# Kernel tuning notes

Hardware: AMD Instinct MI355X
Metric: run time of the kernel (lower is better)

The kernel has to match this reference:

```python
import jax, jax.numpy as jnp
import numpy as np

EPS = 1e-5

def _layernorm(x, w, b):
    mu = jnp.mean(x, axis=-1, keepdims=True)
    var = jnp.mean(jnp.square(x - mu), axis=-1, keepdims=True)
    return (x - mu) * jax.lax.rsqrt(var + EPS) * w + b

def setup_inputs() -> dict:
    key = jax.random.key(0)
    ks = jax.random.split(key, 8)
    B, N, C, D = 32, 1024, 4096, 64
    x = jax.random.normal(ks[0], (B, N, C), dtype=jnp.float32)
    gumbel = jax.random.gumbel(ks[1], (B, N, 2), dtype=jnp.float32)
    ln_w = jnp.ones((C,), jnp.float32)
    ln_b = jnp.zeros((C,), jnp.float32)
    w1 = jax.random.normal(ks[2], (C, D), dtype=jnp.float32) * 0.02
    b1 = jnp.zeros((D,), jnp.float32)
    w2 = jax.random.normal(ks[3], (D, 2), dtype=jnp.float32) * 0.02
    b2 = jnp.zeros((2,), jnp.float32)
    return {"x": x, "gumbel": gumbel, "ln_w": ln_w, "ln_b": ln_b,
            "w1": w1, "b1": b1, "w2": w2, "b2": b2}

def reference(x, gumbel, ln_w, ln_b, w1, b1, w2, b2):
    B, N, C = x.shape
    xn = _layernorm(x, ln_w, ln_b)
    local_x = xn[:, :, : C // 2]                      # [B, N, C/2]
    # policy is all-ones -> weighted mean over tokens
    global_x = jnp.mean(xn[:, :, C // 2:], axis=1, keepdims=True)  # [B, 1, C/2]
    feat = jnp.concatenate(
        [local_x, jnp.broadcast_to(global_x, local_x.shape)], axis=-1)  # [B, N, C]
    h = jax.nn.gelu(feat @ w1 + b1, approximate=False)  # [B, N, 64]
    logits = h @ w2 + b2                                # [B, N, 2]
    pred_score = jax.nn.log_softmax(logits, axis=-1)
    # gumbel-softmax (tau=1, hard=True) with straight-through estimator
    y_soft = jax.nn.softmax(pred_score + gumbel, axis=-1)
    hard = jax.nn.one_hot(jnp.argmax(y_soft, axis=-1), 2, dtype=y_soft.dtype)
    y = hard - jax.lax.stop_gradient(y_soft) + y_soft
    keep = y[:, :, 0]                                   # [B, N]
    # dense equivalent of masked_select/split: zero out dropped tokens
    return x * keep[:, :, None]
```

## Files before the change

kernel.cpp:

```cpp
#include <hip/hip_runtime.h>
#include <math.h>

#define B_   32
#define N_   1024
#define C_   4096
#define HC_  2048
#define D_   64
#define NT_  32768
#define BKC_ 64
#define NCH_ (HC_ / BKC_)
#define AST_ 68

__device__ __forceinline__ float4 ld4(const float* p) {
    return *reinterpret_cast<const float4*>(p);
}

__global__ __launch_bounds__(256) void mk1(
        const float* __restrict__ x, const float* __restrict__ lnw,
        const float* __restrict__ lnb, const float* __restrict__ w1,
        float* __restrict__ Pp, float* __restrict__ muv,
        float* __restrict__ rsv, float* __restrict__ part) {
    __shared__ float smem[8448];
    __shared__ float sLow[64], qLow[64];
    float* As = smem;
    float* Bsm = smem + 4352;

    const int t = threadIdx.x;
    const int tid = blockIdx.x;
    const int T0 = tid * 64;
    const int row = t >> 2;
    const int fq = t & 3;
    const int lane = t & 63, w = t >> 6;
    const int rt = lane >> 3, dt = lane & 7;

    float acc[64];
#pragma unroll
    for (int i = 0; i < 64; ++i) acc[i] = 0.f;
    float sR = 0.f, qR = 0.f;

    float4 xv[4];
    float4 wv[4];
    float lw[4];
    {
        const float* rp = x + (size_t)(T0 + row) * C_ + fq * 16;
#pragma unroll
        for (int i = 0; i < 4; ++i) xv[i] = ld4(rp + i * 4);
        const float4* s4 = reinterpret_cast<const float4*>(w1);
#pragma unroll
        for (int i = 0; i < 4; ++i) {
            wv[i] = s4[i * 256 + t];
            lw[i] = lnw[(i * 256 + t) >> 4];
        }
    }

#pragma unroll 1
    for (int c = 0; c < NCH_; ++c) {
#pragma unroll
        for (int i = 0; i < 4; ++i) {
            const float4 v = xv[i];
            const int kl = fq * 16 + i * 4;
            As[(kl + 0) * AST_ + row] = v.x;
            As[(kl + 1) * AST_ + row] = v.y;
            As[(kl + 2) * AST_ + row] = v.z;
            As[(kl + 3) * AST_ + row] = v.w;
            sR += (v.x + v.y) + (v.z + v.w);
            qR = fmaf(v.x, v.x, fmaf(v.y, v.y,
                 fmaf(v.z, v.z, fmaf(v.w, v.w, qR))));
        }
        {
            float4* b4 = reinterpret_cast<float4*>(Bsm);
#pragma unroll
            for (int i = 0; i < 4; ++i) {
                float4 v = wv[i];
                v.x *= lw[i]; v.y *= lw[i]; v.z *= lw[i]; v.w *= lw[i];
                b4[i * 256 + t] = v;
            }
        }
        __syncthreads();
        if (c + 1 < NCH_) {
            const int k1 = (c + 1) * BKC_;
            const float* rp = x + (size_t)(T0 + row) * C_ + k1 + fq * 16;
#pragma unroll
            for (int i = 0; i < 4; ++i) xv[i] = ld4(rp + i * 4);
            const float4* s4 = reinterpret_cast<const float4*>(
                w1 + (size_t)k1 * D_);
#pragma unroll
            for (int i = 0; i < 4; ++i) {
                wv[i] = s4[i * 256 + t];
                lw[i] = lnw[k1 + ((i * 256 + t) >> 4)];
            }
        }
#pragma unroll 8
        for (int kk = 0; kk < 16; ++kk) {
            const int k = w * 16 + kk;
            const float4 a0 = *reinterpret_cast<const float4*>(
                As + k * AST_ + rt * 8);
            const float4 a1 = *reinterpret_cast<const float4*>(
                As + k * AST_ + rt * 8 + 4);
            const float4 b0 = *reinterpret_cast<const float4*>(
                Bsm + k * 64 + dt * 8);
            const float4 b1 = *reinterpret_cast<const float4*>(
                Bsm + k * 64 + dt * 8 + 4);
            const float av[8] = {a0.x, a0.y, a0.z, a0.w,
                                 a1.x, a1.y, a1.z, a1.w};
            const float bv[8] = {b0.x, b0.y, b0.z, b0.w,
                                 b1.x, b1.y, b1.z, b1.w};
#pragma unroll
            for (int ri = 0; ri < 8; ++ri)
#pragma unroll
                for (int cj = 0; cj < 8; ++cj)
                    acc[ri * 8 + cj] =
                        fmaf(av[ri], bv[cj], acc[ri * 8 + cj]);
        }
        __syncthreads();
    }
    sR += __shfl_xor(sR, 1); qR += __shfl_xor(qR, 1);
    sR += __shfl_xor(sR, 2); qR += __shfl_xor(qR, 2);
    if (fq == 0) { sLow[row] = sR; qLow[row] = qR; }

#pragma unroll
    for (int h = 0; h < 2; ++h) {
#pragma unroll
        for (int i = 0; i < 32; ++i) smem[i * 256 + t] = acc[h * 32 + i];
        __syncthreads();
        if ((w >> 1) == h) {
#pragma unroll
            for (int r2 = 0; r2 < 2; ++r2) {
                const int rowO = rt * 8 + w * 2 + r2;
                float v[8];
#pragma unroll
                for (int cj = 0; cj < 8; ++cj) {
                    const int i = (w - 2 * h) * 16 + r2 * 8 + cj;
                    v[cj] = (smem[i * 256 + lane]
                             + smem[i * 256 + 64 + lane])
                          + (smem[i * 256 + 128 + lane]
                             + smem[i * 256 + 192 + lane]);
                }
                float* dst = Pp + (size_t)(T0 + rowO) * D_ + dt * 8;
                *reinterpret_cast<float4*>(dst) =
                    make_float4(v[0], v[1], v[2], v[3]);
                *reinterpret_cast<float4*>(dst + 4) =
                    make_float4(v[4], v[5], v[6], v[7]);
            }
        }
        __syncthreads();
    }

    float4 wvu[8], bvu[8], gacc[8];
#pragma unroll
    for (int m = 0; m < 8; ++m) {
        wvu[m] = ld4(lnw + HC_ + (m * 64 + lane) * 4);
        bvu[m] = ld4(lnb + HC_ + (m * 64 + lane) * 4);
        gacc[m] = make_float4(0.f, 0.f, 0.f, 0.f);
    }
    for (int i = 0; i < 16; ++i) {
        const int r = w * 16 + i;
        const int tok = T0 + r;
        const float* rowp = x + (size_t)tok * C_ + HC_;
        float4 v[8];
        float s = 0.f, q = 0.f;
#pragma unroll
        for (int m = 0; m < 8; ++m) {
            v[m] = ld4(rowp + (m * 64 + lane) * 4);
            s += (v[m].x + v[m].y) + (v[m].z + v[m].w);
            q = fmaf(v[m].x, v[m].x, fmaf(v[m].y, v[m].y,
                fmaf(v[m].z, v[m].z, fmaf(v[m].w, v[m].w, q))));
        }
#pragma unroll
        for (int o = 1; o < 64; o <<= 1) {
            s += __shfl_xor(s, o);
            q += __shfl_xor(q, o);
        }
        const float S_ = s + sLow[r];
        const float Q_ = q + qLow[r];
        const float mu = S_ * (1.f / C_);
        const float rs = rsqrtf(Q_ * (1.f / C_) - mu * mu + 1e-5f);
        if (lane == 0) {
            muv[tok] = mu;
            rsv[tok] = rs;
        }
#pragma unroll
        for (int m = 0; m < 8; ++m) {
            gacc[m].x += (v[m].x - mu) * rs * wvu[m].x + bvu[m].x;
            gacc[m].y += (v[m].y - mu) * rs * wvu[m].y + bvu[m].y;
            gacc[m].z += (v[m].z - mu) * rs * wvu[m].z + bvu[m].z;
            gacc[m].w += (v[m].w - mu) * rs * wvu[m].w + bvu[m].w;
        }
    }
    float (*sh)[HC_] = reinterpret_cast<float(*)[HC_]>(smem);
    __syncthreads();
#pragma unroll
    for (int m = 0; m < 8; ++m)
        *reinterpret_cast<float4*>(&sh[w][(m * 64 + lane) * 4]) = gacc[m];
    __syncthreads();
    float* pp = part + (size_t)tid * HC_;
#pragma unroll
    for (int m = 0; m < 8; ++m) {
        const int j = (m * 64 + lane) * 4;
        const float4 a0 = ld4(&sh[0][j]);
        const float4 a1 = ld4(&sh[1][j]);
        const float4 a2 = ld4(&sh[2][j]);
        const float4 a3 = ld4(&sh[3][j]);
        float4 r;
        r.x = (a0.x + a1.x) + (a2.x + a3.x);
        r.y = (a0.y + a1.y) + (a2.y + a3.y);
        r.z = (a0.z + a1.z) + (a2.z + a3.z);
        r.w = (a0.w + a1.w) + (a2.w + a3.w);
        if (w == (m & 3))
            *reinterpret_cast<float4*>(pp + j) = r;
    }
}

__global__ __launch_bounds__(256) void k2a_part(
        const float* __restrict__ part, const float* __restrict__ w1,
        const float* __restrict__ lnw, const float* __restrict__ lnb,
        float* __restrict__ gpart, float* __restrict__ Wpart,
        float* __restrict__ Bpart) {
    __shared__ float Gs[256];
    __shared__ float red[512];
    const int t = threadIdx.x;
    const int d = t & 63, s = t >> 6;
    const int blk = blockIdx.x;
    if (blk < 256) {
        const int b = blk >> 3, jq = blk & 7;
        const int j = jq * 256 + t;
        float a = 0.f;
        for (int k = 0; k < 16; ++k)
            a += part[(size_t)(b * 16 + k) * HC_ + j];
        Gs[t] = a;
        __syncthreads();
        float acc = 0.f;
        const int j0 = jq * 256 + s * 64;
        for (int jj = 0; jj < 64; ++jj)
            acc = fmaf(Gs[s * 64 + jj],
                       w1[(size_t)(HC_ + j0 + jj) * D_ + d], acc);
        red[s * 64 + d] = acc;
        __syncthreads();
        if (s == 0)
            gpart[(size_t)blk * 64 + d] =
                red[d] + red[64 + d] + red[128 + d] + red[192 + d];
    } else {
        const int wq = blk - 256;
        const int c0 = wq * 256 + s * 64;
        float a = 0.f, c2 = 0.f;
        for (int c = c0; c < c0 + 64; ++c) {
            const float wvv = w1[(size_t)c * D_ + d];
            a = fmaf(lnw[c], wvv, a);
            c2 = fmaf(lnb[c], wvv, c2);
        }
        red[s * 64 + d] = a;
        red[256 + s * 64 + d] = c2;
        __syncthreads();
        if (s == 0) {
            Wpart[wq * 64 + d] =
                red[d] + red[64 + d] + red[128 + d] + red[192 + d];
            Bpart[wq * 64 + d] = red[256 + d] + red[320 + d]
                               + red[384 + d] + red[448 + d];
        }
    }
}

__global__ __launch_bounds__(256) void k45_decide_mask(
        const float* __restrict__ Pp, const float* __restrict__ muv,
        const float* __restrict__ rsv, const float* __restrict__ gpart,
        const float* __restrict__ Wpart, const float* __restrict__ Bpart,
        const float* __restrict__ b1, const float* __restrict__ w2,
        const float* __restrict__ b2, const float* __restrict__ gum,
        const float* __restrict__ x, float* __restrict__ out) {
    const int t = threadIdx.x;
    const int lane = t & 63, w = t >> 6;
    const int token = (8191 - blockIdx.x) * 4 + w;
    const int b = token >> 10;

    float W1 = 0.f, Bsv = 0.f, gt = 0.f;
#pragma unroll
    for (int q = 0; q < 8; ++q) {
        W1 += Wpart[q * 64 + lane];
        Bsv += Bpart[q * 64 + lane];
        gt += gpart[(size_t)(b * 8 + q) * 64 + lane];
    }
    gt *= (1.f / N_);

    const float2 gv = *reinterpret_cast<const float2*>(gum + token * 2);
    const float p = Pp[(size_t)token * D_ + lane];
    const float mu = muv[token], rs = rsv[token];
    float h = rs * (p - mu * W1) + Bsv + gt + b1[lane];
    h = 0.5f * h * (1.f + erff(h * 0.70710678118654752f));
    const float2 w2v = *reinterpret_cast<const float2*>(w2 + lane * 2);
    float l0 = h * w2v.x;
    float l1 = h * w2v.y;
#pragma unroll
    for (int o = 1; o < 64; o <<= 1) {
        l0 += __shfl_xor(l0, o);
        l1 += __shfl_xor(l1, o);
    }
    const float z0 = l0 + b2[0] + gv.x;
    const float z1 = l1 + b2[1] + gv.y;

    float4* dst = reinterpret_cast<float4*>(out + (size_t)token * C_);
    if (z0 >= z1) {
        const float4* src =
            reinterpret_cast<const float4*>(x + (size_t)token * C_);
#pragma unroll
        for (int c = 0; c < 16; ++c)
            dst[c * 64 + lane] = src[c * 64 + lane];
    } else {
        const float4 z = make_float4(0.f, 0.f, 0.f, 0.f);
#pragma unroll
        for (int c = 0; c < 16; ++c)
            dst[c * 64 + lane] = z;
    }
}

extern "C" void kernel_launch(void* const* d_in, const int* in_sizes, int n_in,
                              void* d_out, int out_size, void* d_ws,
                              size_t ws_size, hipStream_t stream) {
    const float* x   = (const float*)d_in[0];
    const float* gum = (const float*)d_in[1];
    const float* lnw = (const float*)d_in[2];
    const float* lnb = (const float*)d_in[3];
    const float* w1  = (const float*)d_in[4];
    const float* b1  = (const float*)d_in[5];
    const float* w2  = (const float*)d_in[6];
    const float* b2  = (const float*)d_in[7];
    float* out = (float*)d_out;

    float* wsf   = (float*)d_ws;
    float* Pp    = wsf;
    float* muv   = Pp + (size_t)NT_ * D_;
    float* rsv   = muv + NT_;
    float* part  = rsv + NT_;
    float* gpart = part + (size_t)512 * HC_;
    float* Wpart = gpart + 256 * 64;
    float* Bpart = Wpart + 8 * 64;

    mk1<<<512, 256, 0, stream>>>(x, lnw, lnb, w1, Pp, muv, rsv, part);
    k2a_part<<<264, 256, 0, stream>>>(part, w1, lnw, lnb,
                                      gpart, Wpart, Bpart);
    k45_decide_mask<<<NT_ / 4, 256, 0, stream>>>(Pp, muv, rsv, gpart,
                                                 Wpart, Bpart, b1, w2, b2,
                                                 gum, x, out);
}
```

Before: 369.6 us.

## Double-buffer LDS tiles in the projection GEMM and merge the split-K reduction

Splits the shared-memory A/B tiles into two buffers so the next chunk is written to LDS while the current one is being multiplied. This removes one barrier per K-chunk and moves global prefetch two chunks ahead. The cross-wave accumulator reduction now uses the larger LDS in one pass instead of two halves, and the mask kernel walks tokens forward instead of in reverse. Doubling LDS to about 66KB per block may lower occupancy, and keeping two chunks of prefetch live adds register pressure.

```diff
diff --git a/kernel.cpp b/kernel.cpp
--- a/kernel.cpp
+++ b/kernel.cpp
@@ -10,6 +10,7 @@
 #define BKC_ 64
 #define NCH_ (HC_ / BKC_)
 #define AST_ 68
+#define BUF_ 8448
 
 __device__ __forceinline__ float4 ld4(const float* p) {
     return *reinterpret_cast<const float4*>(p);
@@ -20,10 +21,8 @@
         const float* __restrict__ lnb, const float* __restrict__ w1,
         float* __restrict__ Pp, float* __restrict__ muv,
         float* __restrict__ rsv, float* __restrict__ part) {
-    __shared__ float smem[8448];
+    __shared__ float smem[16896];
     __shared__ float sLow[64], qLow[64];
-    float* As = smem;
-    float* Bsm = smem + 4352;
 
     const int t = threadIdx.x;
     const int tid = blockIdx.x;
@@ -41,6 +40,7 @@
     float4 xv[4];
     float4 wv[4];
     float lw[4];
+
     {
         const float* rp = x + (size_t)(T0 + row) * C_ + fq * 16;
 #pragma unroll
@@ -51,24 +51,22 @@
             wv[i] = s4[i * 256 + t];
             lw[i] = lnw[(i * 256 + t) >> 4];
         }
-    }
-
-#pragma unroll 1
-    for (int c = 0; c < NCH_; ++c) {
+        float* A0 = smem;
+        float* B0 = smem + 4352;
 #pragma unroll
         for (int i = 0; i < 4; ++i) {
             const float4 v = xv[i];
             const int kl = fq * 16 + i * 4;
-            As[(kl + 0) * AST_ + row] = v.x;
-            As[(kl + 1) * AST_ + row] = v.y;
-            As[(kl + 2) * AST_ + row] = v.z;
-            As[(kl + 3) * AST_ + row] = v.w;
+            A0[(kl + 0) * AST_ + row] = v.x;
+            A0[(kl + 1) * AST_ + row] = v.y;
+            A0[(kl + 2) * AST_ + row] = v.z;
+            A0[(kl + 3) * AST_ + row] = v.w;
             sR += (v.x + v.y) + (v.z + v.w);
             qR = fmaf(v.x, v.x, fmaf(v.y, v.y,
                  fmaf(v.z, v.z, fmaf(v.w, v.w, qR))));
         }
         {
-            float4* b4 = reinterpret_cast<float4*>(Bsm);
+            float4* b4 = reinterpret_cast<float4*>(B0);
 #pragma unroll
             for (int i = 0; i < 4; ++i) {
                 float4 v = wv[i];
@@ -76,31 +74,37 @@
                 b4[i * 256 + t] = v;
             }
         }
-        __syncthreads();
-        if (c + 1 < NCH_) {
-            const int k1 = (c + 1) * BKC_;
-            const float* rp = x + (size_t)(T0 + row) * C_ + k1 + fq * 16;
-#pragma unroll
-            for (int i = 0; i < 4; ++i) xv[i] = ld4(rp + i * 4);
-            const float4* s4 = reinterpret_cast<const float4*>(
-                w1 + (size_t)k1 * D_);
-#pragma unroll
-            for (int i = 0; i < 4; ++i) {
-                wv[i] = s4[i * 256 + t];
-                lw[i] = lnw[k1 + ((i * 256 + t) >> 4)];
-            }
-        }
+        const float* rp1 = x + (size_t)(T0 + row) * C_ + BKC_ + fq * 16;
+#pragma unroll
+        for (int i = 0; i < 4; ++i) xv[i] = ld4(rp1 + i * 4);
+        const float4* s41 = reinterpret_cast<const float4*>(
+            w1 + (size_t)BKC_ * D_);
+#pragma unroll
+        for (int i = 0; i < 4; ++i) {
+            wv[i] = s41[i * 256 + t];
+            lw[i] = lnw[BKC_ + ((i * 256 + t) >> 4)];
+        }
+        __syncthreads();
+    }
+
+#pragma unroll 1
+    for (int c = 0; c < NCH_; ++c) {
+        float* Acur = smem + (c & 1) * BUF_;
+        float* Bcur = Acur + 4352;
+        float* Anxt = smem + ((c + 1) & 1) * BUF_;
+        float* Bnxt = Anxt + 4352;
+
 #pragma unroll 8
         for (int kk = 0; kk < 16; ++kk) {
             const int k = w * 16 + kk;
             const float4 a0 = *reinterpret_cast<const float4*>(
-                As + k * AST_ + rt * 8);
+                Acur + k * AST_ + rt * 8);
             const float4 a1 = *reinterpret_cast<const float4*>(
-                As + k * AST_ + rt * 8 + 4);
+                Acur + k * AST_ + rt * 8 + 4);
             const float4 b0 = *reinterpret_cast<const float4*>(
-                Bsm + k * 64 + dt * 8);
+                Bcur + k * 64 + dt * 8);
             const float4 b1 = *reinterpret_cast<const float4*>(
-                Bsm + k * 64 + dt * 8 + 4);
+                Bcur + k * 64 + dt * 8 + 4);
             const float av[8] = {a0.x, a0.y, a0.z, a0.w,
                                  a1.x, a1.y, a1.z, a1.w};
             const float bv[8] = {b0.x, b0.y, b0.z, b0.w,
@@ -112,6 +116,40 @@
                     acc[ri * 8 + cj] =
                         fmaf(av[ri], bv[cj], acc[ri * 8 + cj]);
         }
+        if (c + 1 < NCH_) {
+#pragma unroll
+            for (int i = 0; i < 4; ++i) {
+                const float4 v = xv[i];
+                const int kl = fq * 16 + i * 4;
+                Anxt[(kl + 0) * AST_ + row] = v.x;
+                Anxt[(kl + 1) * AST_ + row] = v.y;
+                Anxt[(kl + 2) * AST_ + row] = v.z;
+                Anxt[(kl + 3) * AST_ + row] = v.w;
+                sR += (v.x + v.y) + (v.z + v.w);
+                qR = fmaf(v.x, v.x, fmaf(v.y, v.y,
+                     fmaf(v.z, v.z, fmaf(v.w, v.w, qR))));
+            }
+            float4* b4 = reinterpret_cast<float4*>(Bnxt);
+#pragma unroll
+            for (int i = 0; i < 4; ++i) {
+                float4 v = wv[i];
+                v.x *= lw[i]; v.y *= lw[i]; v.z *= lw[i]; v.w *= lw[i];
+                b4[i * 256 + t] = v;
+            }
+        }
+        if (c + 2 < NCH_) {
+            const int k2 = (c + 2) * BKC_;
+            const float* rp = x + (size_t)(T0 + row) * C_ + k2 + fq * 16;
+#pragma unroll
+            for (int i = 0; i < 4; ++i) xv[i] = ld4(rp + i * 4);
+            const float4* s4 = reinterpret_cast<const float4*>(
+                w1 + (size_t)k2 * D_);
+#pragma unroll
+            for (int i = 0; i < 4; ++i) {
+                wv[i] = s4[i * 256 + t];
+                lw[i] = lnw[k2 + ((i * 256 + t) >> 4)];
+            }
+        }
         __syncthreads();
     }
     sR += __shfl_xor(sR, 1); qR += __shfl_xor(qR, 1);
@@ -119,32 +157,27 @@
     if (fq == 0) { sLow[row] = sR; qLow[row] = qR; }
 
 #pragma unroll
-    for (int h = 0; h < 2; ++h) {
-#pragma unroll
-        for (int i = 0; i < 32; ++i) smem[i * 256 + t] = acc[h * 32 + i];
-        __syncthreads();
-        if ((w >> 1) == h) {
-#pragma unroll
-            for (int r2 = 0; r2 < 2; ++r2) {
-                const int rowO = rt * 8 + w * 2 + r2;
-                float v[8];
-#pragma unroll
-                for (int cj = 0; cj < 8; ++cj) {
-                    const int i = (w - 2 * h) * 16 + r2 * 8 + cj;
-                    v[cj] = (smem[i * 256 + lane]
-                             + smem[i * 256 + 64 + lane])
-                          + (smem[i * 256 + 128 + lane]
-                             + smem[i * 256 + 192 + lane]);
-                }
-                float* dst = Pp + (size_t)(T0 + rowO) * D_ + dt * 8;
-                *reinterpret_cast<float4*>(dst) =
-                    make_float4(v[0], v[1], v[2], v[3]);
-                *reinterpret_cast<float4*>(dst + 4) =
-                    make_float4(v[4], v[5], v[6], v[7]);
-            }
-        }
-        __syncthreads();
-    }
+    for (int i = 0; i < 64; ++i) smem[i * 256 + t] = acc[i];
+    __syncthreads();
+#pragma unroll
+    for (int r2 = 0; r2 < 2; ++r2) {
+        const int rowO = rt * 8 + w * 2 + r2;
+        float v[8];
+#pragma unroll
+        for (int cj = 0; cj < 8; ++cj) {
+            const int i = w * 16 + r2 * 8 + cj;
+            v[cj] = (smem[i * 256 + lane]
+                     + smem[i * 256 + 64 + lane])
+                  + (smem[i * 256 + 128 + lane]
+                     + smem[i * 256 + 192 + lane]);
+        }
+        float* dst = Pp + (size_t)(T0 + rowO) * D_ + dt * 8;
+        *reinterpret_cast<float4*>(dst) =
+            make_float4(v[0], v[1], v[2], v[3]);
+        *reinterpret_cast<float4*>(dst + 4) =
+            make_float4(v[4], v[5], v[6], v[7]);
+    }
+    __syncthreads();
 
     float4 wvu[8], bvu[8], gacc[8];
 #pragma unroll
@@ -269,7 +302,7 @@
         const float* __restrict__ x, float* __restrict__ out) {
     const int t = threadIdx.x;
     const int lane = t & 63, w = t >> 6;
-    const int token = (8191 - blockIdx.x) * 4 + w;
+    const int token = blockIdx.x * 4 + w;
     const int b = token >> 10;
 
     float W1 = 0.f, Bsv = 0.f, gt = 0.f;
```

New measurement: 336.8 us. 8.9% less time.
